# Performance work log

Hardware: AMD Instinct MI355X
Metric: run time of the kernel (lower is better)

## Reference

```python
import jax, jax.numpy as jnp
import numpy as np
import math

B, T, D = 2, 2048, 2048
H, KV, Dh = 16, 4, 128
REP = H // KV
WINDOW = 1024
META = 128
ROPE_BASE = 10000.0


def _apply_rotary(x, pos):
    # x: (B, h, T, Dh), pos: (T,) -- interleaved (even/odd) RoPE as in the torch module
    dh = x.shape[-1]
    inv = 1.0 / (ROPE_BASE ** (jnp.arange(0, dh, 2, dtype=jnp.float32) / dh))  # (Dh/2,)
    freqs = pos.astype(jnp.float32)[:, None] * inv[None, :]                    # (T, Dh/2)
    cos = jnp.cos(freqs)[None, None].astype(x.dtype)
    sin = jnp.sin(freqs)[None, None].astype(x.dtype)
    x1, x2 = x[..., ::2], x[..., 1::2]
    o1 = x1 * cos - x2 * sin
    o2 = x1 * sin + x2 * cos
    return jnp.stack([o1, o2], axis=-1).reshape(x.shape)


def setup_inputs() -> dict:
    key = jax.random.key(0)
    ks = jax.random.split(key, 5)
    s = 0.02
    return {
        "x": jax.random.normal(ks[0], (B, T, D), jnp.float32),
        "Wq": jax.random.normal(ks[1], (D, H * Dh), jnp.float32) * s,
        "Wk": jax.random.normal(ks[2], (D, KV * Dh), jnp.float32) * s,
        "Wv": jax.random.normal(ks[3], (D, KV * Dh), jnp.float32) * s,
        "Wo": jax.random.normal(ks[4], (H * Dh, D), jnp.float32) * s,
    }


def reference(x, Wq, Wk, Wv, Wo):
    Bx, Tx, _ = x.shape
    # projections + head split: q (B,H,T,Dh); k,v (B,KV,T,Dh)
    q = (x @ Wq).reshape(Bx, Tx, H, Dh).transpose(0, 2, 1, 3)
    k = (x @ Wk).reshape(Bx, Tx, KV, Dh).transpose(0, 2, 1, 3)
    v = (x @ Wv).reshape(Bx, Tx, KV, Dh).transpose(0, 2, 1, 3)
    pos = jnp.arange(Tx)
    q = _apply_rotary(q, pos)
    k = _apply_rotary(k, pos)
    # GQA: repeat kv heads (expand+reshape == contiguous repeat along head axis)
    k_full = jnp.repeat(k, REP, axis=1)
    v_full = jnp.repeat(v, REP, axis=1)
    # sliding window: keep META meta tokens + last w content tokens
    w = min(WINDOW, Tx - META)
    k_full = jnp.concatenate([k_full[:, :, :META], k_full[:, :, Tx - w:]], axis=2)
    v_full = jnp.concatenate([v_full[:, :, :META], v_full[:, :, Tx - w:]], axis=2)
    Tk = META + w
    scores = jnp.einsum("bhqd,bhkd->bhqk", q, k_full) / math.sqrt(Dh)
    # torch: triu(full(-inf,(T,Tk)), diagonal=1) added to scores
    mask = jnp.arange(Tk)[None, :] > jnp.arange(Tx)[:, None]   # (T, Tk)
    scores = jnp.where(mask[None, None], -jnp.inf, scores)
    attn = jax.nn.softmax(scores, axis=-1)
    out = jnp.einsum("bhqk,bhkd->bhqd", attn, v_full)
    out = out.transpose(0, 2, 1, 3).reshape(Bx, Tx, H * Dh)
    return out @ Wo
```

## Files before the change

kernel.cpp:

```cpp
#include <hip/hip_runtime.h>
#include <hip/hip_bf16.h>
#include <math.h>

typedef __attribute__((ext_vector_type(4))) float f32x4;
typedef __attribute__((ext_vector_type(8))) short bf16x8;

#define LDSP(p)  ((__attribute__((address_space(3))) void*)(p))
#define GMEMP(p) ((const __attribute__((address_space(1))) void*)(p))

__device__ __forceinline__ short f2b(float f) {
  __hip_bfloat16 h = __float2bfloat16(f);
  return __builtin_bit_cast(short, h);
}
__device__ __forceinline__ float b2f(short s) {
  __hip_bfloat16 h = __builtin_bit_cast(__hip_bfloat16, s);
  return __bfloat162float(h);
}
__device__ __forceinline__ unsigned pack2(float a, float b) {
  return (unsigned)(unsigned short)f2b(a) | ((unsigned)(unsigned short)f2b(b) << 16);
}
__device__ __forceinline__ float exp2_fast(float x) {
  float r;
  asm("v_exp_f32 %0, %1" : "=v"(r) : "v"(x));
  return r;
}

__global__ void cvt_kernel(const float* __restrict__ src, short* __restrict__ dst, int n8) {
  int i = blockIdx.x * blockDim.x + threadIdx.x;
  if (i >= n8) return;
  const float4* s4 = (const float4*)src;
  float4 a = s4[2 * i], b = s4[2 * i + 1];
  bf16x8 o;
  o[0] = f2b(a.x); o[1] = f2b(a.y); o[2] = f2b(a.z); o[3] = f2b(a.w);
  o[4] = f2b(b.x); o[5] = f2b(b.y); o[6] = f2b(b.z); o[7] = f2b(b.w);
  *(bf16x8*)(dst + (size_t)i * 8) = o;
}

__global__ void transpose_all(const float* __restrict__ Wq, const float* __restrict__ Wk,
                              const float* __restrict__ Wv, const float* __restrict__ Wo,
                              short* __restrict__ wqkv_t, short* __restrict__ wo_t) {
  __shared__ float tile[32][33];
  int gx = blockIdx.x;
  const float* src; short* dst; int cols, cx;
  if (gx < 64)       { src = Wq; dst = wqkv_t;                        cols = 2048; cx = gx; }
  else if (gx < 80)  { src = Wk; dst = wqkv_t + (size_t)2048 * 2048;  cols = 512;  cx = gx - 64; }
  else if (gx < 96)  { src = Wv; dst = wqkv_t + (size_t)2560 * 2048;  cols = 512;  cx = gx - 80; }
  else               { src = Wo; dst = wo_t;                          cols = 2048; cx = gx - 96; }
  int c0 = cx * 32, r0 = blockIdx.y * 32;
  int tx = threadIdx.x & 31, ty = threadIdx.x >> 5;
  for (int i = ty; i < 32; i += 8)
    tile[i][tx] = src[(size_t)(r0 + i) * cols + c0 + tx];
  __syncthreads();
  for (int i = ty; i < 32; i += 8)
    dst[(size_t)(c0 + i) * 2048 + r0 + tx] = f2b(tile[tx][i]);
}

template <int OUTBF>
__global__ __launch_bounds__(256) void gemm_bt(const short* __restrict__ A,
                                               const short* __restrict__ Bt,
                                               void* __restrict__ Cv,
                                               int M, int N, int K) {
  __shared__ alignas(16) short As[3][128 * 32];
  __shared__ alignas(16) short Bs[3][128 * 32];
  const int m0 = blockIdx.y * 128, n0 = blockIdx.x * 128;
  const int wave = threadIdx.x >> 6, lane = threadIdx.x & 63;
  const int g = lane >> 4, cl = lane & 15;
  const int wr = (wave >> 1) * 64, wc = (wave & 1) * 64;
  const int tid = threadIdx.x;
  f32x4 acc[4][4];
#pragma unroll
  for (int i = 0; i < 4; ++i)
#pragma unroll
    for (int j = 0; j < 4; ++j) acc[i][j] = (f32x4){0.f, 0.f, 0.f, 0.f};

  const int e0 = tid * 8;
#define STAGE(kt, s)                                                                        \
  {                                                                                         \
    _Pragma("unroll") for (int c = 0; c < 2; ++c) {                                         \
      int e = c * 2048 + e0;                                                                \
      int r = e >> 5;                                                                       \
      int j = (e >> 3) & 3;                                                                 \
      int col = (kt) + 8 * (j ^ ((r >> 1) & 3));                                            \
      __builtin_amdgcn_global_load_lds(GMEMP(A + (size_t)(m0 + r) * K + col),               \
                                       LDSP(&As[s][e]), 16, 0, 0);                          \
      __builtin_amdgcn_global_load_lds(GMEMP(Bt + (size_t)(n0 + r) * K + col),              \
                                       LDSP(&Bs[s][e]), 16, 0, 0);                          \
    }                                                                                       \
  }

  const int nkt = K >> 5;
  STAGE(0, 0);
  STAGE(32, 1);
  asm volatile("s_waitcnt vmcnt(4)" ::: "memory");
  __builtin_amdgcn_s_barrier();
  asm volatile("" ::: "memory");

  int s = 0;
  for (int t = 0; t < nkt; ++t) {
    if (t + 2 < nkt) {
      int s2 = s + 2; if (s2 >= 3) s2 -= 3;
      STAGE((t + 2) << 5, s2);
    }
    bf16x8 af[4], bfr[4];
#pragma unroll
    for (int i = 0; i < 4; ++i) {
      int R = wr + 16 * i + cl;
      af[i] = *(const bf16x8*)&As[s][R * 32 + 8 * (g ^ ((R >> 1) & 3))];
    }
#pragma unroll
    for (int j = 0; j < 4; ++j) {
      int R = wc + 16 * j + cl;
      bfr[j] = *(const bf16x8*)&Bs[s][R * 32 + 8 * (g ^ ((R >> 1) & 3))];
    }
    __builtin_amdgcn_s_setprio(1);
#pragma unroll
    for (int i = 0; i < 4; ++i)
#pragma unroll
      for (int j = 0; j < 4; ++j)
        acc[i][j] = __builtin_amdgcn_mfma_f32_16x16x32_bf16(af[i], bfr[j], acc[i][j], 0, 0, 0);
    __builtin_amdgcn_s_setprio(0);
    asm volatile("s_waitcnt vmcnt(4)" ::: "memory");
    __builtin_amdgcn_s_barrier();
    asm volatile("" ::: "memory");
    if (++s >= 3) s -= 3;
  }
#undef STAGE
#pragma unroll
  for (int i = 0; i < 4; ++i)
#pragma unroll
    for (int j = 0; j < 4; ++j)
#pragma unroll
      for (int r = 0; r < 4; ++r) {
        int row = m0 + wr + 16 * i + 4 * g + r;
        int col = n0 + wc + 16 * j + cl;
        if (OUTBF)
          ((short*)Cv)[(size_t)row * N + col] = f2b(acc[i][j][r]);
        else
          ((float*)Cv)[(size_t)row * N + col] = acc[i][j][r];
      }
}

__global__ void pp_kernel(const short* __restrict__ qkv, short* __restrict__ qb,
                          short* __restrict__ ksel, short* __restrict__ vt) {
  int blk = blockIdx.x;
  if (blk < 16384) {
    const float SCL = 0.08838834764831845f * 1.4426950408889634f;
    int tid = blk * 256 + threadIdx.x;
    int i = tid & 63;
    int h = (tid >> 6) & 15;
    int row = tid >> 10;
    int t = row & 2047;
    int b = row >> 11;
    unsigned u = *(const unsigned*)(qkv + (size_t)row * 3072 + h * 128 + 2 * i);
    float x1 = b2f((short)(u & 0xffff));
    float x2 = b2f((short)(u >> 16));
    float inv = exp2f(-0.20762050593046f * (float)i);
    float ang = (float)t * inv;
    float sn, cs;
    __sincosf(ang, &sn, &cs);
    unsigned w = pack2((x1 * cs - x2 * sn) * SCL, (x1 * sn + x2 * cs) * SCL);
    *(unsigned*)(qb + (size_t)((b * 16 + h) * 2048 + t) * 128 + 2 * i) = w;
  } else if (blk < 16384 + 4096) {
    int tid = (blk - 16384) * 256 + threadIdx.x;
    int i = tid & 63;
    int kvh = (tid >> 6) & 3;
    int row = tid >> 8;
    int t = row & 2047;
    int b = row >> 11;
    int idx = t < 128 ? t : (t >= 1024 ? t - 896 : -1);
    if (idx < 0) return;
    unsigned u = *(const unsigned*)(qkv + (size_t)row * 3072 + 2048 + kvh * 128 + 2 * i);
    float x1 = b2f((short)(u & 0xffff));
    float x2 = b2f((short)(u >> 16));
    float inv = exp2f(-0.20762050593046f * (float)i);
    float ang = (float)t * inv;
    float sn, cs;
    __sincosf(ang, &sn, &cs);
    unsigned w = pack2(x1 * cs - x2 * sn, x1 * sn + x2 * cs);
    *(unsigned*)(ksel + (size_t)((b * 4 + kvh) * 1152 + idx) * 128 + 2 * i) = w;
  } else {
    int tid = (blk - 20480) * 256 + threadIdx.x;
    int idx = tid % 1152;
    int rest = tid / 1152;
    int d = rest & 127;
    int kvh = (rest >> 7) & 3;
    int b = rest >> 9;
    int t = idx < 128 ? idx : idx + 896;
    vt[(size_t)((b * 4 + kvh) * 128 + d) * 1152 + idx] =
        qkv[(size_t)(b * 2048 + t) * 3072 + 2560 + kvh * 128 + d];
  }
}

__global__ __launch_bounds__(256) void attn_kernel(const short* __restrict__ qb,
                                                   const short* __restrict__ ksel,
                                                   const short* __restrict__ vt,
                                                   short* __restrict__ ao) {
  __shared__ alignas(16) short Ksm[2][8192];
  __shared__ alignas(16) short Vsm[2][8192];
  __shared__ alignas(16) short Psm[4][16][72];

  const int blk = blockIdx.x;
  const int qt = 31 - (blk >> 5);
  const int h = blk & 15, b = (blk >> 4) & 1;
  const int kv = h >> 2;
  const int wave = threadIdx.x >> 6, lane = threadIdx.x & 63;
  const int g = lane >> 4, cl = lane & 15;
  const int q0w = qt * 64 + wave * 16;
  const int qi = q0w + cl;
  const int niter = (qt + 1 < 18) ? (qt + 1) : 18;
  const int nfull = (qt < 18) ? qt : 18;

  const short* kselb = ksel + (size_t)(b * 4 + kv) * 1152 * 128;
  const short* vtb = vt + (size_t)(b * 4 + kv) * 128 * 1152;

  const short* qrow = qb + (size_t)((b * 16 + h) * 2048 + qi) * 128;
  bf16x8 qf[4];
#pragma unroll
  for (int d = 0; d < 4; ++d) qf[d] = *(const bf16x8*)(qrow + d * 32 + 8 * g);

  f32x4 o[8];
#pragma unroll
  for (int c = 0; c < 8; ++c) o[c] = (f32x4){0.f, 0.f, 0.f, 0.f};
  float m_i = -1e30f, l_i = 0.f;

#define STAGEK(kk0, buf)                                                                  \
  {                                                                                       \
    _Pragma("unroll") for (int i = 0; i < 4; ++i) {                                       \
      int base = i * 2048 + wave * 512;                                                   \
      int Lel = base + lane * 8;                                                          \
      int kr = Lel >> 7;                                                                  \
      int kc = (Lel & 127) ^ ((kr & 7) << 3);                                             \
      __builtin_amdgcn_global_load_lds(GMEMP(kselb + (size_t)((kk0) + kr) * 128 + kc),    \
                                       LDSP(&Ksm[buf][base]), 16, 0, 0);                  \
    }                                                                                     \
  }
#define STAGEV(kk0, buf)                                                                  \
  {                                                                                       \
    _Pragma("unroll") for (int i = 0; i < 4; ++i) {                                       \
      int base = i * 2048 + wave * 512;                                                   \
      int Lel = base + lane * 8;                                                          \
      int vr = Lel >> 6;                                                                  \
      int vc = (Lel & 63) ^ ((vr & 7) << 3);                                              \
      __builtin_amdgcn_global_load_lds(GMEMP(vtb + (size_t)vr * 1152 + (kk0) + vc),       \
                                       LDSP(&Vsm[buf][base]), 16, 0, 0);                  \
    }                                                                                     \
  }

  STAGEK(0, 0);
  STAGEV(0, 0);
  asm volatile("s_waitcnt vmcnt(0)" ::: "memory");
  __builtin_amdgcn_s_barrier();
  asm volatile("" ::: "memory");

  for (int t = 0; t < niter; ++t) {
    const int cur = t & 1;
    const int kk0 = t * 64;
    if (t + 1 < niter) {
      STAGEK(kk0 + 64, cur ^ 1);
      STAGEV(kk0 + 64, cur ^ 1);
    }

    f32x4 sf[4];
#pragma unroll
    for (int j = 0; j < 4; ++j) sf[j] = (f32x4){0.f, 0.f, 0.f, 0.f};
    const short* kb = &Ksm[cur][0];
    const int sw = (cl & 7) << 3;
    __builtin_amdgcn_s_setprio(1);
#pragma unroll
    for (int j = 0; j < 4; ++j) {
      const int rs = (16 * j + cl) * 128;
#pragma unroll
      for (int d = 0; d < 4; ++d) {
        bf16x8 kf = *(const bf16x8*)&kb[rs + ((d * 32 + 8 * g) ^ sw)];
        sf[j] = __builtin_amdgcn_mfma_f32_16x16x32_bf16(kf, qf[d], sf[j], 0, 0, 0);
      }
    }
    __builtin_amdgcn_s_setprio(0);

    if (t >= nfull) {
#pragma unroll
      for (int j = 0; j < 4; ++j)
#pragma unroll
        for (int r = 0; r < 4; ++r) {
          int key = kk0 + 16 * j + 4 * g + r;
          sf[j][r] = (key <= qi) ? sf[j][r] : -3.0e38f;
        }
    }

    float ma = fmaxf(fmaxf(fmaxf(sf[0][0], sf[0][1]), sf[0][2]), sf[0][3]);
    float mb = fmaxf(fmaxf(fmaxf(sf[1][0], sf[1][1]), sf[1][2]), sf[1][3]);
    float mc = fmaxf(fmaxf(fmaxf(sf[2][0], sf[2][1]), sf[2][2]), sf[2][3]);
    float md = fmaxf(fmaxf(fmaxf(sf[3][0], sf[3][1]), sf[3][2]), sf[3][3]);
    float mx = fmaxf(fmaxf(ma, mb), fmaxf(mc, md));
    mx = fmaxf(mx, __shfl_xor(mx, 16));
    mx = fmaxf(mx, __shfl_xor(mx, 32));

    if (!__all(mx <= m_i + 8.0f)) {
      const float mnew = fmaxf(m_i, mx);
      const float alpha = exp2_fast(m_i - mnew);
      m_i = mnew;
      l_i *= alpha;
#pragma unroll
      for (int c = 0; c < 8; ++c)
#pragma unroll
        for (int r = 0; r < 4; ++r) o[c][r] *= alpha;
    }

    float p[4][4];
#pragma unroll
    for (int j = 0; j < 4; ++j)
#pragma unroll
      for (int r = 0; r < 4; ++r) p[j][r] = exp2_fast(sf[j][r] - m_i);
    float ls = ((p[0][0] + p[0][1]) + (p[0][2] + p[0][3])) +
               ((p[1][0] + p[1][1]) + (p[1][2] + p[1][3])) +
               ((p[2][0] + p[2][1]) + (p[2][2] + p[2][3])) +
               ((p[3][0] + p[3][1]) + (p[3][2] + p[3][3]));
    ls += __shfl_xor(ls, 16);
    ls += __shfl_xor(ls, 32);
    l_i += ls;
    uint4 wA, wB;
    wA.x = pack2(p[0][0], p[0][1]); wA.y = pack2(p[0][2], p[0][3]);
    wA.z = pack2(p[1][0], p[1][1]); wA.w = pack2(p[1][2], p[1][3]);
    wB.x = pack2(p[2][0], p[2][1]); wB.y = pack2(p[2][2], p[2][3]);
    wB.z = pack2(p[3][0], p[3][1]); wB.w = pack2(p[3][2], p[3][3]);
    *(uint4*)&Psm[wave][cl][16 * g] = wA;
    *(uint4*)&Psm[wave][cl][16 * g + 8] = wB;

    asm volatile("s_waitcnt lgkmcnt(0)" ::: "memory");
    const int S0 = 32 * (g & 1) + 4 * (g >> 1);
    uint2 a0 = *(const uint2*)&Psm[wave][cl][S0];
    uint2 a1 = *(const uint2*)&Psm[wave][cl][S0 + 16];
    uint2 b0 = *(const uint2*)&Psm[wave][cl][S0 + 8];
    uint2 b1 = *(const uint2*)&Psm[wave][cl][S0 + 24];
    uint4 u0; u0.x = a0.x; u0.y = a0.y; u0.z = a1.x; u0.w = a1.y;
    uint4 u1; u1.x = b0.x; u1.y = b0.y; u1.z = b1.x; u1.w = b1.y;
    bf16x8 pb0 = __builtin_bit_cast(bf16x8, u0);
    bf16x8 pb1 = __builtin_bit_cast(bf16x8, u1);
    const short* vb = &Vsm[cur][0];
    __builtin_amdgcn_s_setprio(1);
#pragma unroll
    for (int c = 0; c < 8; ++c) {
      const int rvs = (c * 16 + cl) * 64;
      bf16x8 v0 = *(const bf16x8*)&vb[rvs + ((8 * g) ^ sw)];
      bf16x8 v1 = *(const bf16x8*)&vb[rvs + ((32 + 8 * g) ^ sw)];
      o[c] = __builtin_amdgcn_mfma_f32_16x16x32_bf16(v0, pb0, o[c], 0, 0, 0);
      o[c] = __builtin_amdgcn_mfma_f32_16x16x32_bf16(v1, pb1, o[c], 0, 0, 0);
    }
    __builtin_amdgcn_s_setprio(0);

    asm volatile("s_waitcnt vmcnt(0)" ::: "memory");
    __builtin_amdgcn_s_barrier();
    asm volatile("" ::: "memory");
  }
#undef STAGEK
#undef STAGEV

  short* Ol = &Ksm[0][0] + wave * 2176;
  const float invl = 1.0f / l_i;
#pragma unroll
  for (int c = 0; c < 8; ++c) {
    uint2 w;
    w.x = pack2(o[c][0] * invl, o[c][1] * invl);
    w.y = pack2(o[c][2] * invl, o[c][3] * invl);
    *(uint2*)&Ol[cl * 136 + c * 16 + 4 * g] = w;
  }
  asm volatile("s_waitcnt lgkmcnt(0)" ::: "memory");
  const int rowq = lane & 15, seg = lane >> 4;
  const short* srcl = Ol + rowq * 136 + seg * 32;
  short* dst = ao + (size_t)(b * 2048 + q0w + rowq) * 2048 + h * 128 + seg * 32;
#pragma unroll
  for (int k = 0; k < 4; ++k)
    *(bf16x8*)(dst + 8 * k) = *(const bf16x8*)(srcl + 8 * k);
}

extern "C" void kernel_launch(void* const* d_in, const int* in_sizes, int n_in,
                              void* d_out, int out_size, void* d_ws, size_t ws_size,
                              hipStream_t stream) {
  const float* x = (const float*)d_in[0];
  const float* Wq = (const float*)d_in[1];
  const float* Wk = (const float*)d_in[2];
  const float* Wv = (const float*)d_in[3];
  const float* Wo = (const float*)d_in[4];
  float* out = (float*)d_out;

  char* ws = (char*)d_ws;
  short* x_bf = (short*)ws;   ws += (size_t)4096 * 2048 * 2;
  short* wqkv_t = (short*)ws; ws += (size_t)3072 * 2048 * 2;
  short* wo_t = (short*)ws;   ws += (size_t)2048 * 2048 * 2;
  short* qkv = (short*)ws;    ws += (size_t)4096 * 3072 * 2;
  short* q_bf = (short*)ws;   ws += (size_t)2 * 16 * 2048 * 128 * 2;
  short* k_sel = (short*)ws;  ws += (size_t)2 * 4 * 1152 * 128 * 2;
  short* v_t = (short*)ws;    ws += (size_t)2 * 4 * 128 * 1152 * 2;
  short* ao = (short*)ws;     ws += (size_t)4096 * 2048 * 2;

  cvt_kernel<<<4096, 256, 0, stream>>>(x, x_bf, 1048576);
  transpose_all<<<dim3(160, 64), 256, 0, stream>>>(Wq, Wk, Wv, Wo, wqkv_t, wo_t);
  gemm_bt<1><<<dim3(24, 32), 256, 0, stream>>>(x_bf, wqkv_t, qkv, 4096, 3072, 2048);
  pp_kernel<<<25088, 256, 0, stream>>>(qkv, q_bf, k_sel, v_t);
  attn_kernel<<<1024, 256, 0, stream>>>(q_bf, k_sel, v_t, ao);
  gemm_bt<0><<<dim3(16, 32), 256, 0, stream>>>(ao, wo_t, out, 4096, 2048, 2048);
}
```

Baseline: 313.5 us.

## Use 128-row query tiles with 8 waves sharing K/V and single-buffered V

The attention kernel now runs 512 threads per block, and each block covers 128 query rows instead of 64, so each K/V tile loaded into LDS serves twice as many queries and global K/V traffic is halved. V goes to a single buffer whose load is issued at the start of each iteration and waited on with a partial vmcnt plus a barrier before the PV MFMAs. K keeps double buffering. Each block now has two barriers per iteration. The larger causal tiles do more masked work, and there are fewer blocks (512), which may reduce load balance and occupancy.

```diff
diff --git a/kernel.cpp b/kernel.cpp
--- a/kernel.cpp
+++ b/kernel.cpp
@@ -191,24 +191,24 @@
   }
 }
 
-__global__ __launch_bounds__(256) void attn_kernel(const short* __restrict__ qb,
-                                                   const short* __restrict__ ksel,
-                                                   const short* __restrict__ vt,
-                                                   short* __restrict__ ao) {
-  __shared__ alignas(16) short Ksm[2][8192];
-  __shared__ alignas(16) short Vsm[2][8192];
-  __shared__ alignas(16) short Psm[4][16][72];
+__global__ __launch_bounds__(512, 4) void attn_kernel(const short* __restrict__ qb,
+                                                      const short* __restrict__ ksel,
+                                                      const short* __restrict__ vt,
+                                                      short* __restrict__ ao) {
+  __shared__ alignas(16) short SM[33792];
+  short* Vsm = SM + 16384;
+  short* Psm = SM + 24576;
 
   const int blk = blockIdx.x;
-  const int qt = 31 - (blk >> 5);
+  const int qt = 15 - (blk >> 5);
   const int h = blk & 15, b = (blk >> 4) & 1;
   const int kv = h >> 2;
   const int wave = threadIdx.x >> 6, lane = threadIdx.x & 63;
   const int g = lane >> 4, cl = lane & 15;
-  const int q0w = qt * 64 + wave * 16;
+  const int q0w = qt * 128 + wave * 16;
   const int qi = q0w + cl;
-  const int niter = (qt + 1 < 18) ? (qt + 1) : 18;
-  const int nfull = (qt < 18) ? qt : 18;
+  const int niter = (2 * qt + 2 < 18) ? (2 * qt + 2) : 18;
+  const int nfull = (2 * qt < 18) ? (2 * qt) : 18;
 
   const short* kselb = ksel + (size_t)(b * 4 + kv) * 1152 * 128;
   const short* vtb = vt + (size_t)(b * 4 + kv) * 128 * 1152;
@@ -225,45 +225,46 @@
 
 #define STAGEK(kk0, buf)                                                                  \
   {                                                                                       \
-    _Pragma("unroll") for (int i = 0; i < 4; ++i) {                                       \
-      int base = i * 2048 + wave * 512;                                                   \
+    _Pragma("unroll") for (int i = 0; i < 2; ++i) {                                       \
+      int base = i * 4096 + wave * 512;                                                   \
       int Lel = base + lane * 8;                                                          \
       int kr = Lel >> 7;                                                                  \
       int kc = (Lel & 127) ^ ((kr & 7) << 3);                                             \
       __builtin_amdgcn_global_load_lds(GMEMP(kselb + (size_t)((kk0) + kr) * 128 + kc),    \
-                                       LDSP(&Ksm[buf][base]), 16, 0, 0);                  \
+                                       LDSP(SM + (buf) * 8192 + base), 16, 0, 0);         \
     }                                                                                     \
   }
-#define STAGEV(kk0, buf)                                                                  \
+#define STAGEV(kk0)                                                                       \
   {                                                                                       \
-    _Pragma("unroll") for (int i = 0; i < 4; ++i) {                                       \
-      int base = i * 2048 + wave * 512;                                                   \
+    _Pragma("unroll") for (int i = 0; i < 2; ++i) {                                       \
+      int base = i * 4096 + wave * 512;                                                   \
       int Lel = base + lane * 8;                                                          \
       int vr = Lel >> 6;                                                                  \
       int vc = (Lel & 63) ^ ((vr & 7) << 3);                                              \
       __builtin_amdgcn_global_load_lds(GMEMP(vtb + (size_t)vr * 1152 + (kk0) + vc),       \
-                                       LDSP(&Vsm[buf][base]), 16, 0, 0);                  \
+                                       LDSP(Vsm + base), 16, 0, 0);                       \
     }                                                                                     \
   }
 
   STAGEK(0, 0);
-  STAGEV(0, 0);
+  STAGEV(0);
   asm volatile("s_waitcnt vmcnt(0)" ::: "memory");
   __builtin_amdgcn_s_barrier();
   asm volatile("" ::: "memory");
 
+  short* Pw = Psm + wave * 1152 + cl * 72;
+
   for (int t = 0; t < niter; ++t) {
     const int cur = t & 1;
     const int kk0 = t * 64;
-    if (t + 1 < niter) {
-      STAGEK(kk0 + 64, cur ^ 1);
-      STAGEV(kk0 + 64, cur ^ 1);
-    }
+    if (t > 0) STAGEV(kk0);
+    const bool lastk = (t + 1 >= niter);
+    if (!lastk) STAGEK(kk0 + 64, cur ^ 1);
 
     f32x4 sf[4];
 #pragma unroll
     for (int j = 0; j < 4; ++j) sf[j] = (f32x4){0.f, 0.f, 0.f, 0.f};
-    const short* kb = &Ksm[cur][0];
+    const short* kb = SM + cur * 8192;
     const int sw = (cl & 7) << 3;
     __builtin_amdgcn_s_setprio(1);
 #pragma unroll
@@ -323,26 +324,32 @@
     wA.z = pack2(p[1][0], p[1][1]); wA.w = pack2(p[1][2], p[1][3]);
     wB.x = pack2(p[2][0], p[2][1]); wB.y = pack2(p[2][2], p[2][3]);
     wB.z = pack2(p[3][0], p[3][1]); wB.w = pack2(p[3][2], p[3][3]);
-    *(uint4*)&Psm[wave][cl][16 * g] = wA;
-    *(uint4*)&Psm[wave][cl][16 * g + 8] = wB;
+    *(uint4*)&Pw[16 * g] = wA;
+    *(uint4*)&Pw[16 * g + 8] = wB;
+
+    if (!lastk)
+      asm volatile("s_waitcnt vmcnt(2)" ::: "memory");
+    else
+      asm volatile("s_waitcnt vmcnt(0)" ::: "memory");
+    __builtin_amdgcn_s_barrier();
+    asm volatile("" ::: "memory");
 
     asm volatile("s_waitcnt lgkmcnt(0)" ::: "memory");
     const int S0 = 32 * (g & 1) + 4 * (g >> 1);
-    uint2 a0 = *(const uint2*)&Psm[wave][cl][S0];
-    uint2 a1 = *(const uint2*)&Psm[wave][cl][S0 + 16];
-    uint2 b0 = *(const uint2*)&Psm[wave][cl][S0 + 8];
-    uint2 b1 = *(const uint2*)&Psm[wave][cl][S0 + 24];
+    uint2 a0 = *(const uint2*)&Pw[S0];
+    uint2 a1 = *(const uint2*)&Pw[S0 + 16];
+    uint2 b0 = *(const uint2*)&Pw[S0 + 8];
+    uint2 b1 = *(const uint2*)&Pw[S0 + 24];
     uint4 u0; u0.x = a0.x; u0.y = a0.y; u0.z = a1.x; u0.w = a1.y;
     uint4 u1; u1.x = b0.x; u1.y = b0.y; u1.z = b1.x; u1.w = b1.y;
     bf16x8 pb0 = __builtin_bit_cast(bf16x8, u0);
     bf16x8 pb1 = __builtin_bit_cast(bf16x8, u1);
-    const short* vb = &Vsm[cur][0];
     __builtin_amdgcn_s_setprio(1);
 #pragma unroll
     for (int c = 0; c < 8; ++c) {
       const int rvs = (c * 16 + cl) * 64;
-      bf16x8 v0 = *(const bf16x8*)&vb[rvs + ((8 * g) ^ sw)];
-      bf16x8 v1 = *(const bf16x8*)&vb[rvs + ((32 + 8 * g) ^ sw)];
+      bf16x8 v0 = *(const bf16x8*)&Vsm[rvs + ((8 * g) ^ sw)];
+      bf16x8 v1 = *(const bf16x8*)&Vsm[rvs + ((32 + 8 * g) ^ sw)];
       o[c] = __builtin_amdgcn_mfma_f32_16x16x32_bf16(v0, pb0, o[c], 0, 0, 0);
       o[c] = __builtin_amdgcn_mfma_f32_16x16x32_bf16(v1, pb1, o[c], 0, 0, 0);
     }
@@ -355,7 +362,7 @@
 #undef STAGEK
 #undef STAGEV
 
-  short* Ol = &Ksm[0][0] + wave * 2176;
+  short* Ol = SM + wave * 2176;
   const float invl = 1.0f / l_i;
 #pragma unroll
   for (int c = 0; c < 8; ++c) {
@@ -397,6 +404,6 @@
   transpose_all<<<dim3(160, 64), 256, 0, stream>>>(Wq, Wk, Wv, Wo, wqkv_t, wo_t);
   gemm_bt<1><<<dim3(24, 32), 256, 0, stream>>>(x_bf, wqkv_t, qkv, 4096, 3072, 2048);
   pp_kernel<<<25088, 256, 0, stream>>>(qkv, q_bf, k_sel, v_t);
-  attn_kernel<<<1024, 256, 0, stream>>>(q_bf, k_sel, v_t, ao);
+  attn_kernel<<<512, 512, 0, stream>>>(q_bf, k_sel, v_t, ao);
   gemm_bt<0><<<dim3(16, 32), 256, 0, stream>>>(ao, wo_t, out, 4096, 2048, 2048);
 }
```

Result: faster. 300.3 us (-4.2%).
